# Performance work log

Hardware: AMD Instinct MI355X
Metric: run time of the kernel (lower is better)

## Reference

```python
import jax, jax.numpy as jnp
import numpy as np
from jax import lax

B, T, H, W, E = 64, 8, 8, 8, 512
REC = 2048


def setup_inputs() -> dict:
    key = jax.random.key(0)
    kx, kwi, kwr = jax.random.split(key, 3)
    x = jax.random.normal(kx, (B, T, H, W, E), dtype=jnp.float32)
    W_input = jax.random.normal(kwi, (E, REC), dtype=jnp.float32) / np.sqrt(E)
    W_recurrent = jax.random.normal(kwr, (REC, REC), dtype=jnp.float32) / np.sqrt(REC)
    return {"x": x, "W_input": W_input, "W_recurrent": W_recurrent}


def reference(x, W_input, W_recurrent):
    b, t, h, w, e = x.shape
    R = t * h * w
    rec = W_recurrent.shape[0]
    k = int(rec * 0.4)  # 819, matches torch: int(recurrent_size * 0.4)
    x_seq = jnp.swapaxes(x.reshape(b, R, e), 0, 1)  # [R, B, E]
    row_idx = jnp.arange(b)[:, None]

    def step(r, inp):
        z = r @ W_recurrent                    # [B, REC]
        vals, idx = lax.top_k(z, k)            # [B, k]
        s = jnp.zeros_like(z).at[row_idx, idx].set(vals)  # scatter top-k back
        r_new = jnp.tanh(inp @ W_input + s)
        r_new = r_new / (jnp.linalg.norm(r_new, axis=-1, keepdims=True) + 1e-6)
        return r_new, None

    r0 = jnp.zeros((b, rec), dtype=x.dtype)
    r_final, _ = lax.scan(step, r0, x_seq)
    return r_final
```

## Files before the change

### kernel.cpp

```cpp
#include <hip/hip_runtime.h>

#define NSTEP 512
#define EDIM  512
#define REC   2048
#define NB    64
#define KSEL  819
#define KC    8
#define ZCH   256
#define AP    264
#define CSTR  16896
#define WITC  1048576

typedef unsigned short u16;
typedef __bf16 bf16x8 __attribute__((ext_vector_type(8)));
typedef float  f32x4  __attribute__((ext_vector_type(4)));
typedef unsigned long long ull;

static __device__ __forceinline__ f32x4 mfma16(bf16x8 a, bf16x8 b, f32x4 c) {
    return __builtin_amdgcn_mfma_f32_16x16x32_bf16(a, b, c, 0, 0, 0);
}

static __device__ __forceinline__ void split2(float v, u16& c0, u16& c1) {
    __bf16 b0 = (__bf16)v;
    __bf16 b1 = (__bf16)(v - (float)b0);
    c0 = __builtin_bit_cast(u16, b0);
    c1 = __builtin_bit_cast(u16, b1);
}

static __device__ __forceinline__ void cstore4f(float* p, float v) {
    __hip_atomic_store((unsigned*)p, __float_as_uint(v), __ATOMIC_RELAXED, __HIP_MEMORY_SCOPE_AGENT);
}
static __device__ __forceinline__ void cstore4u(unsigned* p, unsigned v) {
    __hip_atomic_store(p, v, __ATOMIC_RELAXED, __HIP_MEMORY_SCOPE_AGENT);
}
static __device__ __forceinline__ unsigned cload4u(const unsigned* p) {
    return __hip_atomic_load(p, __ATOMIC_RELAXED, __HIP_MEMORY_SCOPE_AGENT);
}
static __device__ __forceinline__ void cstore8u(void* p, ull v) {
    __hip_atomic_store((ull*)p, v, __ATOMIC_RELAXED, __HIP_MEMORY_SCOPE_AGENT);
}
static __device__ __forceinline__ ull cload8u(const void* p) {
    return __hip_atomic_load((const ull*)p, __ATOMIC_RELAXED, __HIP_MEMORY_SCOPE_AGENT);
}
static __device__ __forceinline__ float2 cload8f(const float* p) {
    ull u = cload8u(p);
    float2 v; __builtin_memcpy(&v, &u, 8);
    return v;
}

__device__ __forceinline__ void gbarA(unsigned* bar, int bid, int tid,
                                      unsigned gen, bool wait)
{
    __syncthreads();
    if (tid == 0) cstore4u(&bar[bid], gen);
    if (bid == 0 && tid < 64) {
        const ull* sl = (const ull*)bar;
        for (;;) {
            const ull v0 = cload8u(&sl[tid * 2]);
            const ull v1 = cload8u(&sl[tid * 2 + 1]);
            const bool ok = ((unsigned)v0 >= gen) && ((unsigned)(v0 >> 32) >= gen)
                         && ((unsigned)v1 >= gen) && ((unsigned)(v1 >> 32) >= gen);
            if (__all(ok)) break;
            __builtin_amdgcn_s_sleep(1);
        }
        if (tid < 16) cstore4u(&bar[1024 + tid * 32], gen);
    }
    if (wait) {
        if (tid == 0) {
            const int g = bid >> 4;
            while (cload4u(&bar[1024 + g * 32]) < gen)
                __builtin_amdgcn_s_sleep(1);
            __asm__ volatile("" ::: "memory");
        }
        __syncthreads();
    }
}

__device__ __forceinline__ void gbarB(unsigned* bar, int bid, int tid, unsigned gen)
{
    __syncthreads();
    if (bid < NB && tid == 0) cstore4u(&bar[512 + bid], gen);
    if (bid == 0 && tid < 64) {
        for (;;) {
            const unsigned v = cload4u(&bar[512 + tid]);
            if (__all(v >= gen)) break;
            __builtin_amdgcn_s_sleep(1);
        }
        if (tid < 16) cstore4u(&bar[1536 + tid * 32], gen);
    }
    if (tid == 0) {
        const int g = bid >> 4;
        while (cload4u(&bar[1536 + g * 32]) < gen)
            __builtin_amdgcn_s_sleep(1);
        __asm__ volatile("" ::: "memory");
    }
    __syncthreads();
}

__global__ __launch_bounds__(512, 1)
void rnn_persistent(const float* __restrict__ x, const float* __restrict__ Wi,
                    const float* __restrict__ Wr, float* __restrict__ out,
                    u16* __restrict__ rTu, float* __restrict__ zb,
                    u16* __restrict__ Ybf, u16* __restrict__ WiTu,
                    unsigned* __restrict__ bar)
{
    extern __shared__ __align__(16) char smem[];
    u16* WrSu = (u16*)smem;
    u16* aSu  = (u16*)(smem + 67584);
    float* tp = (float*)smem;
    unsigned*      kS    = (unsigned*)(smem + 67584);
    unsigned char* selS  = (unsigned char*)(smem + 67584 + 8192);
    unsigned*      hist  = (unsigned*)(smem + 67584 + 10240);
    __shared__ unsigned s_byte, s_newrem, s_cnteq;
    __shared__ float red[8];

    const int bid = blockIdx.x;
    const int tid = threadIdx.x;
    const int kc = bid & 7, nc = bid >> 3;
    const int n0 = nc * 64, kcbase = kc * ZCH;
    const int wid = tid >> 6, lane = tid & 63;
    const int q = lane >> 4, l16 = lane & 15;
    const int Moff = (wid & 3) * 16, Npair = wid >> 2;
    const bool isB = (bid < NB);
    unsigned* ncnt = &bar[2048];

    {
        const int jt = bid & 31, et = bid >> 5;
        const int j0 = jt * 64, e0 = et * 64;
        const int rr = tid >> 6, ln = tid & 63;
#pragma unroll
        for (int k = 0; k < 8; ++k) {
            const int r = k * 8 + rr;
            tp[r * 65 + ln] = Wi[(long long)(e0 + r) * REC + j0 + ln];
        }
        __syncthreads();
        const int c = tid >> 3, e8 = (tid & 7) * 8;
        u16 h[8], l[8];
#pragma unroll
        for (int i = 0; i < 8; ++i) split2(tp[(e8 + i) * 65 + c], h[i], l[i]);
        ull ph0, ph1, pl0, pl1;
        __builtin_memcpy(&ph0, &h[0], 8); __builtin_memcpy(&ph1, &h[4], 8);
        __builtin_memcpy(&pl0, &l[0], 8); __builtin_memcpy(&pl1, &l[4], 8);
        const long long bI = (long long)(j0 + c) * 512 + e0 + e8;
        cstore8u(&WiTu[bI], ph0);        cstore8u(&WiTu[bI + 4], ph1);
        cstore8u(&WiTu[WITC + bI], pl0); cstore8u(&WiTu[WITC + bI + 4], pl1);
    }
    gbarA(bar, bid, tid, 1u, true);

    {
        const int t0 = bid * 2;
        for (int jc = 0; jc < 32; ++jc) {
            const int j0y = jc * 64;
            f32x4 aY[2][2];
#pragma unroll
            for (int tt = 0; tt < 2; ++tt)
#pragma unroll
                for (int i = 0; i < 2; ++i) aY[tt][i] = (f32x4){0,0,0,0};
            for (int kc2 = 0; kc2 < 2; ++kc2) {
                __syncthreads();
#pragma unroll
                for (int i = 0; i < 8; ++i) {
                    const int chunk = i * 512 + tid;
                    const int cc = chunk >> 11;
                    const int jj = (chunk & 2047) >> 5;
                    const int e8 = chunk & 31;
                    const u16* src = WiTu + (long long)cc * WITC
                                   + (long long)(j0y + jj) * 512 + kc2 * 256 + e8 * 8;
                    const ull w0 = *(const ull*)src;
                    const ull w1 = *(const ull*)(src + 4);
                    u16* dst = WrSu + cc * CSTR + jj * AP + e8 * 8;
                    *(ull*)dst = w0;
                    *(ull*)(dst + 4) = w1;
                }
#pragma unroll
                for (int tt = 0; tt < 2; ++tt) {
                    __syncthreads();
#pragma unroll
                    for (int it = 0; it < 8; ++it) {
                        const int b = it * 8 + wid;
                        const float4 v = *(const float4*)(x
                            + ((long long)b * NSTEP + (t0 + tt)) * EDIM
                            + kc2 * 256 + lane * 4);
                        u16 hh[4], ll[4];
                        split2(v.x, hh[0], ll[0]); split2(v.y, hh[1], ll[1]);
                        split2(v.z, hh[2], ll[2]); split2(v.w, hh[3], ll[3]);
                        ull ph, pl;
                        __builtin_memcpy(&ph, hh, 8); __builtin_memcpy(&pl, ll, 8);
                        *(ull*)&aSu[b * AP + lane * 4] = ph;
                        *(ull*)&aSu[CSTR + b * AP + lane * 4] = pl;
                    }
                    __syncthreads();
                    f32x4 a0 = aY[tt][0], a1 = aY[tt][1];
#pragma unroll
                    for (int ks = 0; ks < 8; ++ks) {
                        const int kk = ks * 32 + q * 8;
                        const u16* ap = aSu + (Moff + l16) * AP + kk;
                        bf16x8 A0 = *(const bf16x8*)(ap);
                        bf16x8 A1 = *(const bf16x8*)(ap + CSTR);
                        const u16* bp0 = WrSu + (Npair * 32 + l16) * AP + kk;
                        bf16x8 B00 = *(const bf16x8*)(bp0);
                        bf16x8 B01 = *(const bf16x8*)(bp0 + CSTR);
                        const u16* bp1 = bp0 + 16 * AP;
                        bf16x8 B10 = *(const bf16x8*)(bp1);
                        bf16x8 B11 = *(const bf16x8*)(bp1 + CSTR);
                        a0 = mfma16(A0, B00, a0);
                        a1 = mfma16(A0, B10, a1);
                        a0 = mfma16(A0, B01, a0);
                        a1 = mfma16(A0, B11, a1);
                        a0 = mfma16(A1, B00, a0);
                        a1 = mfma16(A1, B10, a1);
                    }
                    aY[tt][0] = a0; aY[tt][1] = a1;
                }
            }
            const int jb = j0y + Npair * 32 + l16;
#pragma unroll
            for (int tt = 0; tt < 2; ++tt)
#pragma unroll
                for (int i = 0; i < 4; ++i) {
                    const int row = Moff + q * 4 + i;
                    const unsigned w0 = (unsigned)__builtin_bit_cast(u16, (__bf16)((float*)&aY[tt][0])[i]);
                    const unsigned w1 = (unsigned)__builtin_bit_cast(u16, (__bf16)((float*)&aY[tt][1])[i]);
                    const unsigned o0 = (unsigned)__shfl_xor((int)w0, 1);
                    const unsigned o1 = (unsigned)__shfl_xor((int)w1, 1);
                    if ((lane & 1) == 0) {
                        const long long yb = ((long long)(t0 + tt) * 64 + row) * REC + jb;
                        cstore4u((unsigned*)&Ybf[yb],      w0 | (o0 << 16));
                        cstore4u((unsigned*)&Ybf[yb + 16], w1 | (o1 << 16));
                    }
                }
        }
    }
    {
        const int g = bid * 512 + tid;
        if (g < 65536) cstore8u(rTu + (long long)g * 4, 0ull);
        cstore4f(zb + g, 0.f);
    }
    gbarA(bar, bid, tid, 2u, true);

    {
        for (int it = 0; it < 32; ++it) {
            const int row = it * 8 + wid;
            const int col = lane;
            const float v = Wr[(long long)(kcbase + row) * REC + n0 + col];
            u16 s0, s1; split2(v, s0, s1);
            const int base = col * AP + row;
            WrSu[base] = s0;
            WrSu[CSTR + base] = s1;
        }
        __syncthreads();
    }

    const int hw = tid >> 5, hl = tid & 31;
    for (int t = 0; t < NSTEP; ++t) {
        float* zcur = zb + (size_t)(t & 1) * 131072;
        float* znxt = zb + (size_t)((t + 1) & 1) * 131072;
        cstore4f(znxt + bid * 512 + tid, 0.f);
        {
            ull va[8], vbv[8];
#pragma unroll
            for (int i = 0; i < 8; ++i) {
                const int c = i >> 2;
                const int b = (i & 3) * 16 + hw;
                const u16* src = rTu + (long long)c * 131072 + (long long)b * REC + kcbase + hl * 8;
                va[i] = cload8u(src);
                vbv[i] = cload8u(src + 4);
            }
#pragma unroll
            for (int i = 0; i < 8; ++i) {
                const int c = i >> 2;
                const int b = (i & 3) * 16 + hw;
                u16* dst = aSu + c * CSTR + b * AP + hl * 8;
                *(ull*)dst = va[i];
                *(ull*)(dst + 4) = vbv[i];
            }
        }
        __syncthreads();

        ushort4 yv;
        if (isB) yv = *(const ushort4*)&Ybf[((long long)t * 64 + bid) * REC + tid * 4];

        f32x4 acc0 = {0,0,0,0}, acc1 = {0,0,0,0};
#pragma unroll
        for (int ks = 0; ks < 8; ++ks) {
            const int kk = ks * 32 + q * 8;
            const u16* ap = aSu + (Moff + l16) * AP + kk;
            bf16x8 A0 = *(const bf16x8*)(ap);
            bf16x8 A1 = *(const bf16x8*)(ap + CSTR);
            const u16* bp0 = WrSu + (Npair * 32 + l16) * AP + kk;
            bf16x8 B00 = *(const bf16x8*)(bp0);
            bf16x8 B01 = *(const bf16x8*)(bp0 + CSTR);
            const u16* bp1 = bp0 + 16 * AP;
            bf16x8 B10 = *(const bf16x8*)(bp1);
            bf16x8 B11 = *(const bf16x8*)(bp1 + CSTR);
            acc0 = mfma16(A0, B00, acc0);
            acc1 = mfma16(A0, B10, acc1);
            acc0 = mfma16(A0, B01, acc0);
            acc1 = mfma16(A0, B11, acc1);
            acc0 = mfma16(A1, B00, acc0);
            acc1 = mfma16(A1, B10, acc1);
        }
        {
            const int colA = n0 + Npair * 32 + l16;
#pragma unroll
            for (int i = 0; i < 4; ++i) {
                float* zp = zcur + (long long)(Moff + q * 4 + i) * REC + colA;
                unsafeAtomicAdd(zp,      ((float*)&acc0)[i]);
                unsafeAtomicAdd(zp + 16, ((float*)&acc1)[i]);
            }
        }
        __syncthreads();
        if (tid == 0) atomicAdd(&ncnt[nc << 5], 1u);

        if (isB) {
            const int b = bid;
            const int j0 = tid * 4;
            {
                const unsigned tgt = 8u * (unsigned)(t + 1);
                const unsigned* myc = &ncnt[(tid >> 4) << 5];
                while (cload4u(myc) < tgt) __builtin_amdgcn_s_sleep(1);
                __asm__ volatile("" ::: "memory");
            }
            float zs[4];
            {
                const float2 u0 = cload8f(zcur + (long long)b * REC + j0);
                const float2 u1 = cload8f(zcur + (long long)b * REC + j0 + 2);
                zs[0] = u0.x; zs[1] = u0.y; zs[2] = u1.x; zs[3] = u1.y;
            }
            unsigned kv[4];
#pragma unroll
            for (int s = 0; s < 4; ++s) {
                const unsigned u = __float_as_uint(zs[s]);
                kv[s] = (u & 0x80000000u) ? ~u : (u | 0x80000000u);
            }
            unsigned* hw_ = hist + wid * 256;
            unsigned prefix = 0, remaining = KSEL;
            int done = 0;
            unsigned char sel[4];
            int sel_set = 0;
            for (int byte = 3; byte >= 0 && !done; --byte) {
                {
                    uint4 zz = {0u, 0u, 0u, 0u};
                    *(uint4*)&hw_[lane * 4] = zz;
                }
                const int shift = byte * 8;
                const unsigned pmask = (byte == 3) ? 0u : (0xFFFFFFFFu << (shift + 8));
#pragma unroll
                for (int s = 0; s < 4; ++s) {
                    if ((kv[s] & pmask) == prefix)
                        atomicAdd(&hw_[(kv[s] >> shift) & 255u], 1u);
                }
                __syncthreads();
                if (tid < 64) {
                    unsigned c0 = 0, c1 = 0, c2 = 0, c3 = 0;
#pragma unroll
                    for (int w = 0; w < 8; ++w) {
                        const uint4 hv = *(const uint4*)&hist[w * 256 + tid * 4];
                        c0 += hv.x; c1 += hv.y; c2 += hv.z; c3 += hv.w;
                    }
                    const unsigned tot = c0 + c1 + c2 + c3;
                    unsigned suf = tot;
#pragma unroll
                    for (int st = 1; st < 64; st <<= 1) {
                        unsigned o = __shfl_down(suf, (unsigned)st);
                        if (tid + st >= 64) o = 0u;
                        suf += o;
                    }
                    unsigned S[5];
                    S[0] = suf; S[1] = suf - c0; S[2] = suf - c0 - c1;
                    S[3] = suf - c0 - c1 - c2; S[4] = suf - tot;
                    const unsigned cc[4] = {c0, c1, c2, c3};
#pragma unroll
                    for (int qq = 0; qq < 4; ++qq) {
                        if (S[qq] >= remaining && S[qq + 1] < remaining) {
                            s_byte = (unsigned)(tid * 4 + qq);
                            s_newrem = remaining - S[qq + 1];
                            s_cnteq = cc[qq];
                        }
                    }
                }
                __syncthreads();
                prefix |= (s_byte << shift);
                remaining = s_newrem;
                if (remaining == s_cnteq) { done = 1; continue; }
                if (s_cnteq <= 64u) {
                    const unsigned maskk = 0xFFFFFFFFu << shift;
                    if (tid == 0) kS[128] = 0u;
                    *(unsigned*)&selS[j0] = 0u;
                    __syncthreads();
#pragma unroll
                    for (int s = 0; s < 4; ++s) {
                        if ((kv[s] & maskk) == prefix) {
                            const unsigned p = atomicAdd(&kS[128], 1u);
                            kS[p] = kv[s];
                            kS[64 + p] = (unsigned)(j0 + s);
                        }
                    }
                    __syncthreads();
                    if (tid < 64) {
                        const unsigned cnt = kS[128];
                        if ((unsigned)lane < cnt) {
                            const unsigned myK = kS[lane];
                            const unsigned myI = kS[64 + lane];
                            unsigned rank = 0;
                            for (unsigned j = 0; j < cnt; ++j) {
                                const unsigned bk = kS[j], bi = kS[64 + j];
                                if (bk > myK || (bk == myK && bi < myI)) ++rank;
                            }
                            if (rank < remaining) selS[myI] = 1;
                        }
                    }
                    __syncthreads();
#pragma unroll
                    for (int s = 0; s < 4; ++s) {
                        const unsigned m = kv[s] & maskk;
                        sel[s] = (m > prefix) ? 1 : ((m == prefix) ? selS[j0 + s] : 0);
                    }
                    sel_set = 1;
                    break;
                }
            }
            if (!sel_set) {
                if (done) {
#pragma unroll
                    for (int s = 0; s < 4; ++s)
                        sel[s] = (kv[s] >= prefix) ? 1 : 0;
                } else {
                    *(uint4*)&kS[j0] = *(uint4*)kv;
                    __syncthreads();
                    if (tid == 0) {
                        unsigned rem = remaining;
                        const unsigned T = prefix;
                        for (int j = 0; j < REC; ++j) {
                            const unsigned k = kS[j];
                            unsigned char sl = 0;
                            if (k > T) sl = 1;
                            else if (k == T && rem > 0u) { sl = 1; --rem; }
                            selS[j] = sl;
                        }
                    }
                    __syncthreads();
#pragma unroll
                    for (int s = 0; s < 4; ++s) sel[s] = selS[j0 + s];
                }
            }
            float rn[4]; float ss = 0.f;
            const u16 ya[4] = {yv.x, yv.y, yv.z, yv.w};
#pragma unroll
            for (int s = 0; s < 4; ++s) {
                const float y = __uint_as_float(((unsigned)ya[s]) << 16);
                const float v = y + (sel[s] ? zs[s] : 0.f);
                const float th = tanhf(v);
                rn[s] = th; ss += th * th;
            }
#pragma unroll
            for (int off = 32; off > 0; off >>= 1)
                ss += __shfl_down(ss, (unsigned)off);
            if (lane == 0) red[wid] = ss;
            __syncthreads();
            float a = 0.f;
#pragma unroll
            for (int i = 0; i < 8; ++i) a += red[i];
            const float inv = 1.0f / (sqrtf(a) + 1e-6f);
            u16 o0[4], o1[4];
            float4 ov;
#pragma unroll
            for (int s = 0; s < 4; ++s) {
                const float v = rn[s] * inv;
                split2(v, o0[s], o1[s]);
                ((float*)&ov)[s] = v;
            }
            ull p0, p1;
            __builtin_memcpy(&p0, o0, 8); __builtin_memcpy(&p1, o1, 8);
            cstore8u(rTu + (long long)b * REC + j0, p0);
            cstore8u(rTu + 131072 + (long long)b * REC + j0, p1);
            if (t == NSTEP - 1)
                *(float4*)&out[(long long)b * REC + j0] = ov;
        }
        gbarB(bar, bid, tid, (unsigned)(t + 1));
    }
}

extern "C" void kernel_launch(void* const* d_in, const int* in_sizes, int n_in,
                              void* d_out, int out_size, void* d_ws, size_t ws_size,
                              hipStream_t stream)
{
    const float* x   = (const float*)d_in[0];
    const float* Win = (const float*)d_in[1];
    const float* Wr  = (const float*)d_in[2];
    float* out = (float*)d_out;

    char* ws = (char*)d_ws;
    const size_t BAR = 16384;
    unsigned* bar  = (unsigned*)ws;
    float*    zb   = (float*)(ws + BAR);
    u16*      rTu  = (u16*)(ws + BAR + 2 * 524288);
    u16*      WiTu = (u16*)(ws + BAR + 2 * 524288 + 524288);
    u16*      Ybf  = (u16*)(ws + BAR + 2 * 524288 + 524288 + 4194304);

    static int smem_set = 0;
    if (!smem_set) {
        hipFuncSetAttribute((const void*)rnn_persistent,
                            hipFuncAttributeMaxDynamicSharedMemorySize, 135168);
        smem_set = 1;
    }
    hipMemsetAsync(bar, 0, BAR, stream);
    rnn_persistent<<<256, 512, 135168, stream>>>(x, Win, Wr, out, rTu, zb, Ybf, WiTu, bar);
}
```

Before: 7.181 ms.

## Replace per-step global barrier with group counters and self-zeroing z buffer

Drops the centralized two-level grid barrier at the end of each timestep. Blocks now wait at the start of the next step on four group counters, each bumped by the 16 B-blocks that produce r for that batch group. Zeroing of the next z buffer moves into the B-blocks, which clear z right after reading it, and both buffers are zeroed at init. This is meant to cut barrier latency and the extra round trip through block 0. It relies on careful ordering between z reads, zeroing, and the next step's atomics; stale reads or races are possible if memory ordering is insufficient.

```diff
diff --git a/kernel.cpp b/kernel.cpp
--- a/kernel.cpp
+++ b/kernel.cpp
@@ -74,27 +74,6 @@
         }
         __syncthreads();
     }
-}
-
-__device__ __forceinline__ void gbarB(unsigned* bar, int bid, int tid, unsigned gen)
-{
-    __syncthreads();
-    if (bid < NB && tid == 0) cstore4u(&bar[512 + bid], gen);
-    if (bid == 0 && tid < 64) {
-        for (;;) {
-            const unsigned v = cload4u(&bar[512 + tid]);
-            if (__all(v >= gen)) break;
-            __builtin_amdgcn_s_sleep(1);
-        }
-        if (tid < 16) cstore4u(&bar[1536 + tid * 32], gen);
-    }
-    if (tid == 0) {
-        const int g = bid >> 4;
-        while (cload4u(&bar[1536 + g * 32]) < gen)
-            __builtin_amdgcn_s_sleep(1);
-        __asm__ volatile("" ::: "memory");
-    }
-    __syncthreads();
 }
 
 __global__ __launch_bounds__(512, 1)
@@ -123,6 +102,7 @@
     const int Moff = (wid & 3) * 16, Npair = wid >> 2;
     const bool isB = (bid < NB);
     unsigned* ncnt = &bar[2048];
+    unsigned* gcnt = &bar[1536];
 
     {
         const int jt = bid & 31, et = bid >> 5;
@@ -235,6 +215,7 @@
         const int g = bid * 512 + tid;
         if (g < 65536) cstore8u(rTu + (long long)g * 4, 0ull);
         cstore4f(zb + g, 0.f);
+        cstore4f(zb + 131072 + g, 0.f);
     }
     gbarA(bar, bid, tid, 2u, true);
 
@@ -254,8 +235,12 @@
     const int hw = tid >> 5, hl = tid & 31;
     for (int t = 0; t < NSTEP; ++t) {
         float* zcur = zb + (size_t)(t & 1) * 131072;
-        float* znxt = zb + (size_t)((t + 1) & 1) * 131072;
-        cstore4f(znxt + bid * 512 + tid, 0.f);
+        if (tid < 4) {
+            const unsigned tgt = 16u * (unsigned)t;
+            while (cload4u(&gcnt[tid * 32]) < tgt) __builtin_amdgcn_s_sleep(1);
+        }
+        __asm__ volatile("" ::: "memory");
+        __syncthreads();
         {
             ull va[8], vbv[8];
 #pragma unroll
@@ -323,9 +308,13 @@
             }
             float zs[4];
             {
-                const float2 u0 = cload8f(zcur + (long long)b * REC + j0);
-                const float2 u1 = cload8f(zcur + (long long)b * REC + j0 + 2);
+                float* zp = zcur + (long long)b * REC + j0;
+                const float2 u0 = cload8f(zp);
+                const float2 u1 = cload8f(zp + 2);
                 zs[0] = u0.x; zs[1] = u0.y; zs[2] = u1.x; zs[3] = u1.y;
+                __asm__ volatile("" ::: "memory");
+                cstore8u(zp, 0ull);
+                cstore8u(zp + 2, 0ull);
             }
             unsigned kv[4];
 #pragma unroll
@@ -476,8 +465,9 @@
             cstore8u(rTu + 131072 + (long long)b * REC + j0, p1);
             if (t == NSTEP - 1)
                 *(float4*)&out[(long long)b * REC + j0] = ov;
-        }
-        gbarB(bar, bid, tid, (unsigned)(t + 1));
+            __syncthreads();
+            if (tid == 0) atomicAdd(&gcnt[(b >> 4) * 32], 1u);
+        }
     }
 }
 
```

New measurement: 8.043 ms. 12.0% more time.
